# Optimization experiments

Measured on AMD Instinct MI355X. Metric: run time of the kernel, lower is better.

Reference implementation:

```python
import jax, jax.numpy as jnp
import numpy as np

V, E, H2, T_LEN, B, NTAG = 50257, 512, 1024, 512, 64, 7
H = H2 // 2  # per-direction hidden
START, STOP = 5, 6


def _lstm_dir(x, h0, c0, w_ih, w_hh, b_ih, b_hh, reverse=False):
    # x: [B, T, E]; returns hidden states [B, T, H]
    def step(carry, x_t):
        h, c = carry
        g = x_t @ w_ih.T + b_ih + h @ w_hh.T + b_hh  # [B, 4H]
        i, f, gg, o = jnp.split(g, 4, axis=-1)       # PyTorch gate order i,f,g,o
        c = jax.nn.sigmoid(f) * c + jax.nn.sigmoid(i) * jnp.tanh(gg)
        h = jax.nn.sigmoid(o) * jnp.tanh(c)
        return (h, c), h
    xs = jnp.swapaxes(x, 0, 1)  # [T, B, E]
    _, hs = jax.lax.scan(step, (h0, c0), xs, reverse=reverse)
    return jnp.swapaxes(hs, 0, 1)


def _viterbi(logits, transitions):
    def step(prev, logit_t):  # prev: [B, NTAG]
        v = prev[:, :, None] + transitions[None, :, :]  # [B, prev, next]
        new = logit_t + jnp.max(v, axis=1)
        bp = jnp.argmax(v, axis=1)
        return new, bp
    first = logits[:, 0]
    rest = jnp.swapaxes(logits[:, 1:], 0, 1)  # [T-1, B, NTAG]
    last, bps = jax.lax.scan(step, first, rest)
    scores = jnp.max(last, axis=-1)            # [B]
    last_tag = jnp.argmax(last, axis=-1)       # [B]

    def back(tag, bp_t):  # bp_t: [B, NTAG]
        prev = jnp.take_along_axis(bp_t, tag[:, None], axis=1)[:, 0]
        return prev, prev
    _, earlier = jax.lax.scan(back, last_tag, bps, reverse=True)  # [T-1, B], tags 0..T-2
    paths = jnp.concatenate([jnp.swapaxes(earlier, 0, 1), last_tag[:, None]], axis=1)  # [B, T]
    return scores, paths


def setup_inputs() -> dict:
    key = jax.random.key(0)
    ks = jax.random.split(key, 16)
    s = 1.0 / np.sqrt(H)
    inp = {
        "sentences": jax.random.randint(ks[0], (B, T_LEN), 0, V),
        "emb": jax.random.normal(ks[1], (V, E), jnp.float32),
        "w_ih_f": jax.random.uniform(ks[2], (4 * H, E), jnp.float32, -s, s),
        "w_hh_f": jax.random.uniform(ks[3], (4 * H, H), jnp.float32, -s, s),
        "b_ih_f": jax.random.uniform(ks[4], (4 * H,), jnp.float32, -s, s),
        "b_hh_f": jax.random.uniform(ks[5], (4 * H,), jnp.float32, -s, s),
        "w_ih_b": jax.random.uniform(ks[6], (4 * H, E), jnp.float32, -s, s),
        "w_hh_b": jax.random.uniform(ks[7], (4 * H, H), jnp.float32, -s, s),
        "b_ih_b": jax.random.uniform(ks[8], (4 * H,), jnp.float32, -s, s),
        "b_hh_b": jax.random.uniform(ks[9], (4 * H,), jnp.float32, -s, s),
        "w_out": jax.random.normal(ks[10], (NTAG, H2), jnp.float32) * 0.02,
        "b_out": jnp.zeros((NTAG,), jnp.float32),
        "h0": jax.random.normal(ks[12], (2, B, H), jnp.float32),
        "c0": jax.random.normal(ks[13], (2, B, H), jnp.float32),
    }
    trans = jax.random.normal(ks[14], (NTAG, NTAG), jnp.float32)
    trans = trans.at[START, :].set(-100.0).at[:, STOP].set(-100.0)
    inp["transitions"] = trans
    return inp


def reference(sentences, emb, w_ih_f, w_hh_f, b_ih_f, b_hh_f,
              w_ih_b, w_hh_b, b_ih_b, b_hh_b, w_out, b_out, h0, c0, transitions):
    x = emb[sentences]  # [B, T, E]
    out_f = _lstm_dir(x, h0[0], c0[0], w_ih_f, w_hh_f, b_ih_f, b_hh_f, reverse=False)
    out_b = _lstm_dir(x, h0[1], c0[1], w_ih_b, w_hh_b, b_ih_b, b_hh_b, reverse=True)
    lstm_out = jnp.concatenate([out_f, out_b], axis=-1)  # [B, T, 2H]
    logits = lstm_out @ w_out.T + b_out                  # [B, T, NTAG]
    scores, paths = _viterbi(logits, transitions)
    return scores, paths
```

## Files before the change

### kernel.cpp

```cpp
#include <hip/hip_runtime.h>
#include <cstdint>
#include <cstddef>

#define NTAG 7

typedef unsigned int u32;
typedef unsigned long long u64;
using bf16x8 = __attribute__((ext_vector_type(8))) short;
using f32x4  = __attribute__((ext_vector_type(4))) float;

#define MFMA(A,B,C) __builtin_amdgcn_mfma_f32_16x16x32_bf16((A),(B),(C),0,0,0)

union abf { u64 q[2]; ushort e[8]; bf16x8 v; };

__device__ __forceinline__ u32 rtn_bf16(float f) {
    u32 b = __float_as_uint(f);
    return (b + 0x7fffu + ((b >> 16) & 1u)) >> 16;
}

__global__ __launch_bounds__(256) void prep_w_kernel(
    const float* __restrict__ wif, const float* __restrict__ whf,
    const float* __restrict__ wib, const float* __restrict__ whb,
    ushort* __restrict__ planes)
{
    int f = blockIdx.x * 256 + threadIdx.x;
    int mat = f >> 17;
    int i8 = (f & 0x1FFFF) << 3;
    const float* src = (mat == 0) ? wif : (mat == 1) ? whf : (mat == 2) ? wib : whb;
    float4 v0 = *(const float4*)(src + i8);
    float4 v1 = *(const float4*)(src + i8 + 4);
    ushort o[8];
    const float* pv = (const float*)&v0;
#pragma unroll
    for (int j = 0; j < 4; ++j) o[j] = (ushort)rtn_bf16(pv[j]);
    pv = (const float*)&v1;
#pragma unroll
    for (int j = 0; j < 4; ++j) o[4 + j] = (ushort)rtn_bf16(pv[j]);
    ushort* dst = planes + ((size_t)mat << 20) + i8;
    *(ushort4*)dst = make_ushort4(o[0], o[1], o[2], o[3]);
    *(ushort4*)(dst + 4) = make_ushort4(o[4], o[5], o[6], o[7]);
}

__global__ __launch_bounds__(256) void prep_x_kernel(
    const int* __restrict__ sent, const float* __restrict__ emb,
    ushort* __restrict__ xb)
{
    long f = (long)blockIdx.x * 256 + threadIdx.x;
    long e8 = f << 3;
    int bt = (int)(e8 >> 9);
    int e  = (int)(e8 & 511);
    int tok = sent[bt];
    const float* src = emb + (size_t)tok * 512 + e;
    float4 v0 = *(const float4*)(src);
    float4 v1 = *(const float4*)(src + 4);
    ushort o[8];
    const float* pv = (const float*)&v0;
#pragma unroll
    for (int j = 0; j < 4; ++j) o[j] = (ushort)rtn_bf16(pv[j]);
    pv = (const float*)&v1;
#pragma unroll
    for (int j = 0; j < 4; ++j) o[4 + j] = (ushort)rtn_bf16(pv[j]);
    ushort* dst = xb + e8;
    *(ushort4*)dst = make_ushort4(o[0], o[1], o[2], o[3]);
    *(ushort4*)(dst + 4) = make_ushort4(o[4], o[5], o[6], o[7]);
}

__global__ __launch_bounds__(256, 1) void lstm_mfma_kernel(
    const int* __restrict__ sent, const float* __restrict__ emb,
    const ushort* __restrict__ planes, const ushort* __restrict__ xb,
    const float* __restrict__ bif, const float* __restrict__ bhf,
    const float* __restrict__ bib, const float* __restrict__ bhb,
    const float* __restrict__ wout,
    const float* __restrict__ h0, const float* __restrict__ c0,
    ushort* __restrict__ hglob,
    float* __restrict__ logits,
    float* __restrict__ partial,
    int* __restrict__ flags)
{
    __shared__ __align__(16) ushort hstage[16 * 512];
    __shared__ float sums_s[4 * 16 * 33];
    __shared__ float hv_s[16 * 33];
    __shared__ float bias_s[4 * 32];
    __shared__ float wout_s[7 * 33];

    const int tid = threadIdx.x;
    const int w   = tid >> 6;
    const int L   = tid & 63;
    const int ln  = L & 15;
    const int lk  = L >> 4;
    const int g   = blockIdx.x & 7;
    const int slot= blockIdx.x >> 3;
    const int d   = g & 1;
    const int bq  = g >> 1;
    const int B0  = bq << 4;
    const int u0  = slot << 5;

    const ushort* wip = planes + ((size_t)(d ? 2 : 0) << 20);
    const ushort* whp = planes + ((size_t)(d ? 3 : 1) << 20);

    bf16x8 Bh[2][16];
#pragma unroll
    for (int h = 0; h < 2; ++h) {
        const size_t row = (size_t)(w * 512 + u0 + h * 16 + ln);
#pragma unroll
        for (int kb = 0; kb < 16; ++kb)
            Bh[h][kb] = *(const bf16x8*)(whp + row * 512 + kb * 32 + lk * 8);
    }
    if (tid < 128) {
        int gg = tid >> 5, uu = tid & 31;
        int grow = gg * 512 + u0 + uu;
        bias_s[tid] = d ? (bib[grow] + bhb[grow]) : (bif[grow] + bhf[grow]);
    }
    if (tid < 224) {
        int tg = tid >> 5, uu = tid & 31;
        wout_s[tg * 33 + uu] = wout[(size_t)tg * 1024 + d * 512 + u0 + uu];
    }
    const int cb = tid >> 4, uh = tid & 15;
    float cst[2];
    {
        const float* cr = c0 + ((size_t)(d * 64) + B0 + cb) * 512 + u0 + uh * 2;
        cst[0] = cr[0]; cst[1] = cr[1];
    }
    __syncthreads();

    const int gb = B0 + ln;
    f32x4 xacc0, xacc1;

    auto x_phase = [&](int tnext) {
        f32x4 a0a = {0,0,0,0}, a0b = {0,0,0,0}, a1a = {0,0,0,0}, a1b = {0,0,0,0};
        const size_t row0 = (size_t)(w * 512 + u0 + ln);
        const size_t row1 = row0 + 16;
#pragma unroll
        for (int kb = 0; kb < 16; ++kb) {
            bf16x8 A;
            if (xb) {
                A = *(const bf16x8*)(xb + ((size_t)gb * 512 + tnext) * 512 + kb * 32 + lk * 8);
            } else {
                int tok = sent[gb * 512 + tnext];
                const float* xr = emb + (size_t)tok * 512 + kb * 32 + lk * 8;
                float4 f0 = *(const float4*)(xr);
                float4 f1 = *(const float4*)(xr + 4);
                abf t;
                const float* pv = (const float*)&f0;
#pragma unroll
                for (int j = 0; j < 4; ++j) t.e[j] = (ushort)rtn_bf16(pv[j]);
                pv = (const float*)&f1;
#pragma unroll
                for (int j = 0; j < 4; ++j) t.e[4 + j] = (ushort)rtn_bf16(pv[j]);
                A = t.v;
            }
            bf16x8 Bx0 = *(const bf16x8*)(wip + row0 * 512 + kb * 32 + lk * 8);
            bf16x8 Bx1 = *(const bf16x8*)(wip + row1 * 512 + kb * 32 + lk * 8);
            if (kb & 1) { a0b = MFMA(A, Bx0, a0b); a1b = MFMA(A, Bx1, a1b); }
            else        { a0a = MFMA(A, Bx0, a0a); a1a = MFMA(A, Bx1, a1a); }
        }
        xacc0 = a0a + a0b;
        xacc1 = a1a + a1b;
    };

    x_phase(d ? 511 : 0);

    const char* hsb = (const char*)hstage;
    const int hx = (ln & 7) << 4;

#define AL(P) __hip_atomic_load((P), __ATOMIC_RELAXED, __HIP_MEMORY_SCOPE_AGENT)

    for (int s = 0; s < 512; ++s) {
        const int t = d ? (511 - s) : s;

        if (s > 0 && w == 0) {
            const int* fp = flags + (g << 4) + (L & 15);
            while (true) {
                int v = AL(fp);
                if (__all(v >= s)) break;
                __builtin_amdgcn_s_sleep(1);
            }
        }
        __syncthreads();

        if (s > 0) {
            const u64* hq = (const u64*)(hglob + ((size_t)((s & 1) * 2 + d) * 64 + B0) * 512);
            u64 sv0 = AL(hq + tid * 2);          u64 sv1 = AL(hq + tid * 2 + 1);
            u64 sv2 = AL(hq + 512 + tid * 2);    u64 sv3 = AL(hq + 512 + tid * 2 + 1);
            u64 sv4 = AL(hq + 1024 + tid * 2);   u64 sv5 = AL(hq + 1024 + tid * 2 + 1);
            u64 sv6 = AL(hq + 1536 + tid * 2);   u64 sv7 = AL(hq + 1536 + tid * 2 + 1);
            __builtin_amdgcn_s_waitcnt(0);
            __builtin_amdgcn_sched_barrier(0);
            char* hd = (char*)hstage;
            const int c_ = (tid & 63) * 16;
            const int r_ = tid >> 6;
            {
                int rr = r_;
                char* a = hd + rr * 1024 + (c_ ^ ((rr & 7) << 4));
                *(u64*)a = sv0; *(u64*)(a + 8) = sv1;
            }
            {
                int rr = r_ + 4;
                char* a = hd + rr * 1024 + (c_ ^ ((rr & 7) << 4));
                *(u64*)a = sv2; *(u64*)(a + 8) = sv3;
            }
            {
                int rr = r_ + 8;
                char* a = hd + rr * 1024 + (c_ ^ ((rr & 7) << 4));
                *(u64*)a = sv4; *(u64*)(a + 8) = sv5;
            }
            {
                int rr = r_ + 12;
                char* a = hd + rr * 1024 + (c_ ^ ((rr & 7) << 4));
                *(u64*)a = sv6; *(u64*)(a + 8) = sv7;
            }
        }
        __syncthreads();

        f32x4 f0a = xacc0, f0b = {0,0,0,0}, f1a = xacc1, f1b = {0,0,0,0};
        if (s == 0) {
            const float* hr = h0 + ((size_t)(d * 64) + gb) * 512;
#pragma unroll
            for (int kb = 0; kb < 16; ++kb) {
                float4 q0 = *(const float4*)(hr + kb * 32 + lk * 8);
                float4 q1 = *(const float4*)(hr + kb * 32 + lk * 8 + 4);
                abf A;
                const float* pv = (const float*)&q0;
#pragma unroll
                for (int j = 0; j < 4; ++j) A.e[j] = (ushort)rtn_bf16(pv[j]);
                pv = (const float*)&q1;
#pragma unroll
                for (int j = 0; j < 4; ++j) A.e[4 + j] = (ushort)rtn_bf16(pv[j]);
                if (kb & 1) { f0b = MFMA(A.v, Bh[0][kb], f0b); f1b = MFMA(A.v, Bh[1][kb], f1b); }
                else        { f0a = MFMA(A.v, Bh[0][kb], f0a); f1a = MFMA(A.v, Bh[1][kb], f1a); }
            }
        } else {
            abf A[16];
#pragma unroll
            for (int kb = 0; kb < 16; ++kb)
                A[kb].v = *(const bf16x8*)(hsb + ln * 1024 + ((kb * 64 + lk * 16) ^ hx));
#pragma unroll
            for (int kb = 0; kb < 16; ++kb) {
                if (kb & 1) { f0b = MFMA(A[kb].v, Bh[0][kb], f0b); f1b = MFMA(A[kb].v, Bh[1][kb], f1b); }
                else        { f0a = MFMA(A[kb].v, Bh[0][kb], f0a); f1a = MFMA(A[kb].v, Bh[1][kb], f1a); }
            }
        }
        f32x4 g0 = f0a + f0b, g1 = f1a + f1b;

#pragma unroll
        for (int r = 0; r < 4; ++r) {
            int b = lk * 4 + r;
            sums_s[w * 528 + b * 33 + ln]      = g0[r];
            sums_s[w * 528 + b * 33 + 16 + ln] = g1[r];
        }
        __syncthreads();

        {
            u32 pk = 0;
#pragma unroll
            for (int e = 0; e < 2; ++e) {
                int u = uh * 2 + e;
                float si = sums_s[0 * 528 + cb * 33 + u] + bias_s[u];
                float sf = sums_s[1 * 528 + cb * 33 + u] + bias_s[32 + u];
                float sg = sums_s[2 * 528 + cb * 33 + u] + bias_s[64 + u];
                float so = sums_s[3 * 528 + cb * 33 + u] + bias_s[96 + u];
                float ig = 1.f / (1.f + expf(-si));
                float fg = 1.f / (1.f + expf(-sf));
                float gv = tanhf(sg);
                float og = 1.f / (1.f + expf(-so));
                float cn = fg * cst[e] + ig * gv;
                cst[e] = cn;
                float hh = og * tanhf(cn);
                hv_s[cb * 33 + u] = hh;
                pk |= rtn_bf16(hh) << (16 * e);
            }
            u32* dst = (u32*)(hglob + ((size_t)(((s + 1) & 1) * 2 + d) * 64 + B0 + cb) * 512 + u0 + uh * 2);
            __hip_atomic_store(dst, pk, __ATOMIC_RELAXED, __HIP_MEMORY_SCOPE_AGENT);
        }
        __syncthreads();

        if (tid >= 144) {
            int q = tid - 144, tg = q >> 4, b = q & 15;
            float a = 0.f;
#pragma unroll
            for (int u = 0; u < 32; ++u)
                a = fmaf(hv_s[b * 33 + u], wout_s[tg * 33 + u], a);
            if (partial)
                __builtin_nontemporal_store(a, partial +
                    ((size_t)t * 64 + B0 + b) * 224 + (slot * 2 + d) * 7 + tg);
            else
                atomicAdd(&logits[((size_t)t * 64 + B0 + b) * NTAG + tg], a);
        }

        if (s < 511) x_phase(d ? (510 - s) : (s + 1));

        __builtin_amdgcn_s_waitcnt(0);
        __syncthreads();
        if (s < 511 && tid == 0)
            __hip_atomic_store(flags + (g << 4) + slot, s + 1,
                               __ATOMIC_RELAXED, __HIP_MEMORY_SCOPE_AGENT);
    }
#undef AL
}

__global__ __launch_bounds__(256) void viterbi_kernel(
    const float* __restrict__ logits, const float* __restrict__ partial,
    const float* __restrict__ bout, const float* __restrict__ trans,
    unsigned char* __restrict__ bp,
    float* __restrict__ out)
{
    __shared__ float Ls[4][512][7];
    const int tid = threadIdx.x;
    const int b0 = blockIdx.x << 2;

    if (partial) {
        for (int idx2 = tid; idx2 < 2048; idx2 += 256) {
            int bl = idx2 >> 9, t = idx2 & 511;
            const float* pp = partial + ((size_t)t * 64 + b0 + bl) * 224;
            float a0=0,a1=0,a2=0,a3=0,a4=0,a5=0,a6=0;
#pragma unroll 8
            for (int c = 0; c < 32; ++c) {
                const float* q = pp + c * 7;
                a0 += q[0]; a1 += q[1]; a2 += q[2]; a3 += q[3];
                a4 += q[4]; a5 += q[5]; a6 += q[6];
            }
            Ls[bl][t][0] = a0 + bout[0]; Ls[bl][t][1] = a1 + bout[1];
            Ls[bl][t][2] = a2 + bout[2]; Ls[bl][t][3] = a3 + bout[3];
            Ls[bl][t][4] = a4 + bout[4]; Ls[bl][t][5] = a5 + bout[5];
            Ls[bl][t][6] = a6 + bout[6];
        }
    } else {
        for (int idx = tid; idx < 4 * 512 * 7; idx += 256) {
            int bl = idx / 3584;
            int rem = idx - bl * 3584;
            int t = rem / 7;
            int tg = rem - t * 7;
            Ls[bl][t][tg] = logits[((size_t)t * 64 + b0 + bl) * 7 + tg] + bout[tg];
        }
    }
    __syncthreads();

    const int w = tid >> 6;
    const int lane = tid & 63;
    const int b = b0 + w;
    const int k = lane;

    float tr[7];
#pragma unroll
    for (int j = 0; j < 7; ++j) tr[j] = (k < 7) ? trans[j * 7 + k] : -1e30f;
    float prev = (k < 7) ? Ls[w][0][k] : -1e30f;
    unsigned char* bpb = bp + (size_t)b * 512 * 8;

    for (int t = 1; t < 512; ++t) {
        float best = __shfl(prev, 0, 64) + tr[0];
        int bj = 0;
#pragma unroll
        for (int j = 1; j < 7; ++j) {
            float v = __shfl(prev, j, 64) + tr[j];
            if (v > best) { best = v; bj = j; }
        }
        float lv = (k < 7) ? Ls[w][t][k] : 0.f;
        if (k < 7) bpb[t * 8 + k] = (unsigned char)bj;
        prev = lv + best;
    }

    float pv[7];
#pragma unroll
    for (int j = 0; j < 7; ++j) pv[j] = __shfl(prev, j, 64);
    float best = pv[0]; int bj = 0;
#pragma unroll
    for (int j = 1; j < 7; ++j) if (pv[j] > best) { best = pv[j]; bj = j; }
    if (lane == 0) {
        out[b] = best;
        out[64 + (size_t)b * 512 + 511] = (float)bj;
    }

    int cur = bj;
    for (int tc = 448; tc >= 0; tc -= 64) {
        int t = tc + lane;
        u64 row = *(const u64*)(bpb + (size_t)t * 8);
        for (int i = 63; i >= 0; --i) {
            int t2 = tc + i;
            if (t2 < 1) break;
            u64 r = __shfl(row, i, 64);
            cur = (int)((r >> (cur * 8)) & 0xFF);
            if (lane == 0) out[64 + (size_t)b * 512 + (t2 - 1)] = (float)cur;
        }
    }
}

extern "C" void kernel_launch(void* const* d_in, const int* in_sizes, int n_in,
                              void* d_out, int out_size, void* d_ws, size_t ws_size,
                              hipStream_t stream)
{
    (void)in_sizes; (void)n_in; (void)out_size;
    const int*   sent = (const int*)d_in[0];
    const float* emb  = (const float*)d_in[1];
    const float* wif  = (const float*)d_in[2];
    const float* whf  = (const float*)d_in[3];
    const float* bif  = (const float*)d_in[4];
    const float* bhf  = (const float*)d_in[5];
    const float* wib  = (const float*)d_in[6];
    const float* whb  = (const float*)d_in[7];
    const float* bib  = (const float*)d_in[8];
    const float* bhb  = (const float*)d_in[9];
    const float* wout = (const float*)d_in[10];
    const float* bout = (const float*)d_in[11];
    const float* h0   = (const float*)d_in[12];
    const float* c0   = (const float*)d_in[13];
    const float* trans= (const float*)d_in[14];
    float* out = (float*)d_out;

    char* p = (char*)d_ws;
    float*  logits = (float*)p;            p += 917504;
    int*    flags  = (int*)p;              p += 8192;
    ushort* hglob  = (ushort*)p;           p += 2 * 2 * 64 * 512 * 2;
    unsigned char* bp = (unsigned char*)p; p += 262144;
    ushort* planes = (ushort*)p;           p += 4 * 1048576 * 2;
    size_t base_need = (size_t)(p - (char*)d_ws);
    ushort* xb = nullptr;
    float*  partial = nullptr;
    if (ws_size >= base_need + (size_t)64 * 512 * 512 * 2) {
        xb = (ushort*)p;  p += (size_t)64 * 512 * 512 * 2;
        if (ws_size >= (size_t)(p - (char*)d_ws) + (size_t)512 * 64 * 224 * 4)
            partial = (float*)p;
    }

    hipMemsetAsync(d_ws, 0, 917504 + 8192, stream);
    prep_w_kernel<<<2048, 256, 0, stream>>>(wif, whf, wib, whb, planes);
    if (xb) prep_x_kernel<<<8192, 256, 0, stream>>>(sent, emb, xb);
    lstm_mfma_kernel<<<128, 256, 0, stream>>>(
        sent, emb, planes, xb, bif, bhf, bib, bhb,
        wout, h0, c0, hglob, logits, partial, flags);
    viterbi_kernel<<<16, 256, 0, stream>>>(logits, partial, bout, trans, bp, out);
}
```

Baseline: 5.316 ms.

## Use XCC-local cache-bypass loads for h exchange and move flag signal earlier

At kernel start each block writes its XCC id into a table, and the group checks whether all its cooperating blocks share one XCC while the paired direction sits on a different one. If so, the per-step hidden-state exchange and flag polling use inline global loads/stores with only the sc0 bit instead of agent-scope atomics, aiming to keep the traffic in the shared L2 rather than going further out. The flag store and next x-phase are also moved ahead of the logits partial computation, so dependent blocks are released sooner. This relies on XCC placement and on the cache-coherence behaviour of sc0 bits, and it uses extra flag memory that must be zeroed.

Result: faster. 5.097 ms (-4.1%).

```diff
diff --git a/kernel.cpp b/kernel.cpp
--- a/kernel.cpp
+++ b/kernel.cpp
@@ -8,10 +8,12 @@
 typedef unsigned long long u64;
 using bf16x8 = __attribute__((ext_vector_type(8))) short;
 using f32x4  = __attribute__((ext_vector_type(4))) float;
+using i32x4  = __attribute__((ext_vector_type(4))) int;
 
 #define MFMA(A,B,C) __builtin_amdgcn_mfma_f32_16x16x32_bf16((A),(B),(C),0,0,0)
 
 union abf { u64 q[2]; ushort e[8]; bf16x8 v; };
+union qv  { i32x4 v; u64 q[2]; };
 
 __device__ __forceinline__ u32 rtn_bf16(float f) {
     u32 b = __float_as_uint(f);
@@ -82,6 +84,7 @@
     __shared__ float hv_s[16 * 33];
     __shared__ float bias_s[4 * 32];
     __shared__ float wout_s[7 * 33];
+    __shared__ int   fast_s;
 
     const int tid = threadIdx.x;
     const int w   = tid >> 6;
@@ -121,7 +124,31 @@
         const float* cr = c0 + ((size_t)(d * 64) + B0 + cb) * 512 + u0 + uh * 2;
         cst[0] = cr[0]; cst[1] = cr[1];
     }
+
+    {
+        int xcc = (int)__builtin_amdgcn_s_getreg(20 | (3 << 11));
+        int* tab = flags + 512;
+        if (tid == 0)
+            __hip_atomic_store(tab + (g << 4) + slot, (xcc & 0xF) + 1,
+                               __ATOMIC_RELAXED, __HIP_MEMORY_SCOPE_AGENT);
+        if (w == 0) {
+            const int* myp = tab + (g << 4) + (L & 15);
+            const int* nbp = tab + ((g ^ 1) << 4);
+            const int* pp = (L == 16) ? nbp : myp;
+            int v;
+            while (true) {
+                v = __hip_atomic_load(pp, __ATOMIC_RELAXED, __HIP_MEMORY_SCOPE_AGENT);
+                if (__all(v > 0)) break;
+                __builtin_amdgcn_s_sleep(2);
+            }
+            int v0 = __shfl(v, 0, 64);
+            int vn = __shfl(v, 16, 64);
+            int uni = __all((L < 16) ? (v == v0) : 1);
+            if (L == 0) fast_s = (uni && (v0 != vn)) ? 1 : 0;
+        }
+    }
     __syncthreads();
+    const int fast = fast_s;
 
     const int gb = B0 + ln;
     f32x4 xacc0, xacc1;
@@ -170,21 +197,49 @@
 
         if (s > 0 && w == 0) {
             const int* fp = flags + (g << 4) + (L & 15);
-            while (true) {
-                int v = AL(fp);
-                if (__all(v >= s)) break;
-                __builtin_amdgcn_s_sleep(1);
+            if (fast) {
+                while (true) {
+                    int v;
+                    asm volatile("global_load_dword %0, %1, off sc0\n\t"
+                                 "s_waitcnt vmcnt(0)"
+                                 : "=&v"(v) : "v"(fp) : "memory");
+                    if (__all(v >= s)) break;
+                    __builtin_amdgcn_s_sleep(1);
+                }
+            } else {
+                while (true) {
+                    int v = AL(fp);
+                    if (__all(v >= s)) break;
+                    __builtin_amdgcn_s_sleep(1);
+                }
             }
         }
         __syncthreads();
 
         if (s > 0) {
             const u64* hq = (const u64*)(hglob + ((size_t)((s & 1) * 2 + d) * 64 + B0) * 512);
-            u64 sv0 = AL(hq + tid * 2);          u64 sv1 = AL(hq + tid * 2 + 1);
-            u64 sv2 = AL(hq + 512 + tid * 2);    u64 sv3 = AL(hq + 512 + tid * 2 + 1);
-            u64 sv4 = AL(hq + 1024 + tid * 2);   u64 sv5 = AL(hq + 1024 + tid * 2 + 1);
-            u64 sv6 = AL(hq + 1536 + tid * 2);   u64 sv7 = AL(hq + 1536 + tid * 2 + 1);
-            __builtin_amdgcn_s_waitcnt(0);
+            qv q0, q1, q2, q3;
+            if (fast) {
+                const char* p0 = (const char*)hq + tid * 16;
+                const char* p1 = p0 + 4096;
+                const char* p2 = p0 + 8192;
+                const char* p3 = p0 + 12288;
+                asm volatile(
+                    "global_load_dwordx4 %0, %4, off sc0\n\t"
+                    "global_load_dwordx4 %1, %5, off sc0\n\t"
+                    "global_load_dwordx4 %2, %6, off sc0\n\t"
+                    "global_load_dwordx4 %3, %7, off sc0\n\t"
+                    "s_waitcnt vmcnt(0)"
+                    : "=&v"(q0.v), "=&v"(q1.v), "=&v"(q2.v), "=&v"(q3.v)
+                    : "v"(p0), "v"(p1), "v"(p2), "v"(p3)
+                    : "memory");
+            } else {
+                q0.q[0] = AL(hq + tid * 2);          q0.q[1] = AL(hq + tid * 2 + 1);
+                q1.q[0] = AL(hq + 512 + tid * 2);    q1.q[1] = AL(hq + 512 + tid * 2 + 1);
+                q2.q[0] = AL(hq + 1024 + tid * 2);   q2.q[1] = AL(hq + 1024 + tid * 2 + 1);
+                q3.q[0] = AL(hq + 1536 + tid * 2);   q3.q[1] = AL(hq + 1536 + tid * 2 + 1);
+                __builtin_amdgcn_s_waitcnt(0);
+            }
             __builtin_amdgcn_sched_barrier(0);
             char* hd = (char*)hstage;
             const int c_ = (tid & 63) * 16;
@@ -192,22 +247,22 @@
             {
                 int rr = r_;
                 char* a = hd + rr * 1024 + (c_ ^ ((rr & 7) << 4));
-                *(u64*)a = sv0; *(u64*)(a + 8) = sv1;
+                *(u64*)a = q0.q[0]; *(u64*)(a + 8) = q0.q[1];
             }
             {
                 int rr = r_ + 4;
                 char* a = hd + rr * 1024 + (c_ ^ ((rr & 7) << 4));
-                *(u64*)a = sv2; *(u64*)(a + 8) = sv3;
+                *(u64*)a = q1.q[0]; *(u64*)(a + 8) = q1.q[1];
             }
             {
                 int rr = r_ + 8;
                 char* a = hd + rr * 1024 + (c_ ^ ((rr & 7) << 4));
-                *(u64*)a = sv4; *(u64*)(a + 8) = sv5;
+                *(u64*)a = q2.q[0]; *(u64*)(a + 8) = q2.q[1];
             }
             {
                 int rr = r_ + 12;
                 char* a = hd + rr * 1024 + (c_ ^ ((rr & 7) << 4));
-                *(u64*)a = sv6; *(u64*)(a + 8) = sv7;
+                *(u64*)a = q3.q[0]; *(u64*)(a + 8) = q3.q[1];
             }
         }
         __syncthreads();
@@ -217,13 +272,13 @@
             const float* hr = h0 + ((size_t)(d * 64) + gb) * 512;
 #pragma unroll
             for (int kb = 0; kb < 16; ++kb) {
-                float4 q0 = *(const float4*)(hr + kb * 32 + lk * 8);
-                float4 q1 = *(const float4*)(hr + kb * 32 + lk * 8 + 4);
+                float4 q0f = *(const float4*)(hr + kb * 32 + lk * 8);
+                float4 q1f = *(const float4*)(hr + kb * 32 + lk * 8 + 4);
                 abf A;
-                const float* pv = (const float*)&q0;
+                const float* pv = (const float*)&q0f;
 #pragma unroll
                 for (int j = 0; j < 4; ++j) A.e[j] = (ushort)rtn_bf16(pv[j]);
-                pv = (const float*)&q1;
+                pv = (const float*)&q1f;
 #pragma unroll
                 for (int j = 0; j < 4; ++j) A.e[4 + j] = (ushort)rtn_bf16(pv[j]);
                 if (kb & 1) { f0b = MFMA(A.v, Bh[0][kb], f0b); f1b = MFMA(A.v, Bh[1][kb], f1b); }
@@ -270,9 +325,27 @@
                 pk |= rtn_bf16(hh) << (16 * e);
             }
             u32* dst = (u32*)(hglob + ((size_t)(((s + 1) & 1) * 2 + d) * 64 + B0 + cb) * 512 + u0 + uh * 2);
-            __hip_atomic_store(dst, pk, __ATOMIC_RELAXED, __HIP_MEMORY_SCOPE_AGENT);
+            if (fast)
+                asm volatile("global_store_dword %0, %1, off sc0"
+                             :: "v"(dst), "v"(pk) : "memory");
+            else
+                __hip_atomic_store(dst, pk, __ATOMIC_RELAXED, __HIP_MEMORY_SCOPE_AGENT);
         }
         __syncthreads();
+
+        if (s < 511) x_phase(d ? (510 - s) : (s + 1));
+
+        __builtin_amdgcn_s_waitcnt(0);
+        __syncthreads();
+        if (s < 511 && tid == 0) {
+            int* fsp = flags + (g << 4) + slot;
+            int val = s + 1;
+            if (fast)
+                asm volatile("global_store_dword %0, %1, off sc0"
+                             :: "v"(fsp), "v"(val) : "memory");
+            else
+                __hip_atomic_store(fsp, val, __ATOMIC_RELAXED, __HIP_MEMORY_SCOPE_AGENT);
+        }
 
         if (tid >= 144) {
             int q = tid - 144, tg = q >> 4, b = q & 15;
@@ -286,14 +359,6 @@
             else
                 atomicAdd(&logits[((size_t)t * 64 + B0 + b) * NTAG + tg], a);
         }
-
-        if (s < 511) x_phase(d ? (510 - s) : (s + 1));
-
-        __builtin_amdgcn_s_waitcnt(0);
-        __syncthreads();
-        if (s < 511 && tid == 0)
-            __hip_atomic_store(flags + (g << 4) + slot, s + 1,
-                               __ATOMIC_RELAXED, __HIP_MEMORY_SCOPE_AGENT);
     }
 #undef AL
 }
```
